# Kernel tuning notes

Hardware: AMD Instinct MI355X
Metric: run time of the kernel (lower is better)

The kernel has to match this reference:

```python
import jax, jax.numpy as jnp
import numpy as np

DIM = 2048
N_HEAD = 32
N_KV = 8
HEAD_DIM = DIM // N_HEAD  # 64
GROUP = N_HEAD // N_KV    # 4


def setup_inputs() -> dict:
    key = jax.random.key(0)
    k1, k2, k3, k4 = jax.random.split(key, 4)
    B, S = 2, 2048
    x = jax.random.normal(k1, (B, S, DIM), dtype=jnp.float32)
    freqs_cis = jax.random.normal(k2, (S, HEAD_DIM // 2, 2), dtype=jnp.float32)
    wqkv_w = jax.random.normal(k3, (DIM, (N_HEAD + 2 * N_KV) * HEAD_DIM), dtype=jnp.float32) * 0.02
    wo_w = jax.random.normal(k4, (DIM, DIM), dtype=jnp.float32) * 0.02
    return {"x": x, "freqs_cis": freqs_cis, "wqkv_w": wqkv_w, "wo_w": wo_w}


def apply_rotary_emb(x, freqs_cis):
    # x: (B, S, H, head_dim), freqs_cis: (S, head_dim//2, 2)
    B, S, H, D = x.shape
    xs = x.astype(jnp.float32).reshape(B, S, H, D // 2, 2)
    fc = freqs_cis.reshape(1, S, 1, D // 2, 2)
    real = xs[..., 0] * fc[..., 0] - xs[..., 1] * fc[..., 1]
    imag = xs[..., 1] * fc[..., 0] + xs[..., 0] * fc[..., 1]
    out = jnp.stack([real, imag], axis=-1).reshape(B, S, H, D)
    return out.astype(x.dtype)


def reference(x, freqs_cis, wqkv_w, wo_w):
    B, S, _ = x.shape
    kv_size = N_KV * HEAD_DIM
    qkv = x @ wqkv_w  # (B, S, (n_head+2*n_kv)*head_dim)
    xq = qkv[..., :DIM].reshape(B, S, N_HEAD, HEAD_DIM)
    xk = qkv[..., DIM:DIM + kv_size].reshape(B, S, N_KV, HEAD_DIM)
    xv = qkv[..., DIM + kv_size:].reshape(B, S, N_KV, HEAD_DIM)

    xq = apply_rotary_emb(xq, freqs_cis)
    xk = apply_rotary_emb(xk, freqs_cis)

    # GQA without materializing repeated KV heads:
    # q: (B, n_kv, group, S, d); k, v: (B, n_kv, S, d)
    q = xq.transpose(0, 2, 1, 3).reshape(B, N_KV, GROUP, S, HEAD_DIM)
    k = xk.transpose(0, 2, 1, 3)
    v = xv.transpose(0, 2, 1, 3)

    scale = 1.0 / jnp.sqrt(jnp.asarray(HEAD_DIM, dtype=q.dtype))
    scores = jnp.einsum('bkgqd,bkKd->bkgqK', q, k) * scale  # (B, n_kv, group, S, S)
    causal = jnp.tril(jnp.ones((S, S), dtype=bool))
    neg = jnp.asarray(jnp.finfo(scores.dtype).min, dtype=scores.dtype)
    scores = jnp.where(causal, scores, neg)
    probs = jax.nn.softmax(scores, axis=-1)
    out = jnp.einsum('bkgqK,bkKd->bkgqd', probs, v)  # (B, n_kv, group, S, d)
    out = out.reshape(B, N_HEAD, S, HEAD_DIM).transpose(0, 2, 1, 3).reshape(B, S, DIM)
    return out @ wo_w
```

## Files before the change

### kernel.cpp

```cpp
#include <hip/hip_runtime.h>
#include <hip/hip_bf16.h>
#include <math.h>

#define DIM 2048
#define NH 32
#define NKV 8
#define HD 64
#define SEQ 2048
#define BATCH 2
#define MTOT (BATCH*SEQ)
#define QKV_N ((NH + 2*NKV)*HD)
#define QSCALE 0.18033688011112042f

typedef __bf16 bf16x8 __attribute__((ext_vector_type(8)));
typedef float f32x4 __attribute__((ext_vector_type(4)));

#if __has_builtin(__builtin_amdgcn_exp2f)
#define EXP2F __builtin_amdgcn_exp2f
#else
#define EXP2F exp2f
#endif

__device__ __forceinline__ void gld_lds16(const void* g, void* l) {
  __builtin_amdgcn_global_load_lds((__attribute__((address_space(1))) void*)g,
                                   (__attribute__((address_space(3))) void*)l,
                                   16, 0, 0);
}

__global__ void cvt_x_kernel(const float* __restrict__ src, __hip_bfloat16* __restrict__ dst, int n4) {
  int i = blockIdx.x * 256 + threadIdx.x;
  if (i >= n4) return;
  float4 v = ((const float4*)src)[i];
  union { __hip_bfloat16 h[4]; uint2 u; } t;
  t.h[0] = __float2bfloat16(v.x); t.h[1] = __float2bfloat16(v.y);
  t.h[2] = __float2bfloat16(v.z); t.h[3] = __float2bfloat16(v.w);
  ((uint2*)dst)[i] = t.u;
}

__global__ void transpose_cvt_kernel(const float* __restrict__ src, __hip_bfloat16* __restrict__ dst,
                                     int R, int C) {
  __shared__ float tile[32][33];
  int c0 = blockIdx.x * 32, r0 = blockIdx.y * 32;
  int tx = threadIdx.x & 31, ty = threadIdx.x >> 5;
  #pragma unroll
  for (int i = ty; i < 32; i += 8)
    tile[i][tx] = src[(size_t)(r0 + i) * C + c0 + tx];
  __syncthreads();
  #pragma unroll
  for (int i = ty; i < 32; i += 8)
    dst[(size_t)(c0 + i) * R + r0 + tx] = __float2bfloat16(tile[tx][i]);
}

__global__ __launch_bounds__(128) void gemm_qkv_rope_kernel(const __hip_bfloat16* __restrict__ A,
                                                            const __hip_bfloat16* __restrict__ Bt,
                                                            const float* __restrict__ freqs,
                                                            __hip_bfloat16* __restrict__ Qb,
                                                            __hip_bfloat16* __restrict__ Kb,
                                                            __hip_bfloat16* __restrict__ Vb) {
  __shared__ __hip_bfloat16 As[64 * 32];
  __shared__ __hip_bfloat16 Bs[128 * 32];
  const int tid = threadIdx.x;
  const int w = tid >> 6, lane = tid & 63, ln = lane & 15, quad = lane >> 4;
  const int id = blockIdx.x;
  const int by = (id & 7) * 8 + ((id >> 3) & 7);
  const int bx = id >> 6;
  const int m0 = by * 64, n0 = bx * 128;
  const int K = DIM;
  const __hip_bfloat16* Ag = A + (size_t)(m0 + w * 32 + (lane >> 2)) * K + (lane & 3) * 8;
  const __hip_bfloat16* Bg = Bt + (size_t)(n0 + w * 64 + (lane >> 2)) * K + (lane & 3) * 8;
  __hip_bfloat16* AsW = &As[w * 1024];
  __hip_bfloat16* BsW = &Bs[w * 2048];
  f32x4 acc[4][4] = {};
  for (int k0 = 0; k0 < K; k0 += 32) {
    gld_lds16(Ag + k0, AsW);
    gld_lds16(Ag + (size_t)16 * K + k0, AsW + 512);
    #pragma unroll
    for (int c = 0; c < 4; c++)
      gld_lds16(Bg + (size_t)(c * 16) * K + k0, BsW + c * 512);
    __syncthreads();
    bf16x8 af[4], bf[4];
    #pragma unroll
    for (int i = 0; i < 4; i++)
      af[i] = *(const bf16x8*)&As[(i * 16 + ln) * 32 + quad * 8];
    #pragma unroll
    for (int j = 0; j < 4; j++)
      bf[j] = *(const bf16x8*)&Bs[(w * 64 + j * 16 + ln) * 32 + quad * 8];
    #pragma unroll
    for (int i = 0; i < 4; i++)
      #pragma unroll
      for (int j = 0; j < 4; j++)
        acc[i][j] = __builtin_amdgcn_mfma_f32_16x16x32_bf16(af[i], bf[j], acc[i][j], 0, 0, 0);
    __syncthreads();
  }
  const int region = (n0 >= 2560) ? 2 : (n0 >= 2048 ? 1 : 0);
  #pragma unroll
  for (int i = 0; i < 4; i++) {
    #pragma unroll
    for (int j = 0; j < 4; j++) {
      const int n = n0 + w * 64 + j * 16 + ln;
      const int d = n & 63;
      #pragma unroll
      for (int r = 0; r < 4; r++) {
        const int m = m0 + i * 16 + quad * 4 + r;
        const int bb = m >> 11, s = m & 2047;
        float v = acc[i][j][r];
        if (region == 2) {
          Vb[((size_t)(bb * NKV + ((n - 2560) >> 6)) * SEQ + s) * HD + d] = __float2bfloat16(v);
        } else {
          float p = __shfl_xor(v, 1);
          const float2 fc = *(const float2*)&freqs[s * 64 + (d & ~1)];
          float o = (d & 1) ? (v * fc.x + p * fc.y) : (v * fc.x - p * fc.y);
          if (region == 0)
            Qb[((size_t)(bb * NH + (n >> 6)) * SEQ + s) * HD + d] = __float2bfloat16(o * QSCALE);
          else
            Kb[((size_t)(bb * NKV + ((n - 2048) >> 6)) * SEQ + s) * HD + d] = __float2bfloat16(o);
        }
      }
    }
  }
}

__global__ __launch_bounds__(128) void gemm_wo_kernel(const __hip_bfloat16* __restrict__ A,
                                                      const __hip_bfloat16* __restrict__ Bt,
                                                      float* __restrict__ C) {
  __shared__ __hip_bfloat16 As[64 * 32];
  __shared__ __hip_bfloat16 Bs[128 * 32];
  const int tid = threadIdx.x;
  const int w = tid >> 6, lane = tid & 63, ln = lane & 15, quad = lane >> 4;
  const int id = blockIdx.x;
  const int by = (id & 7) * 8 + ((id >> 3) & 7);
  const int bx = id >> 6;
  const int m0 = by * 64, n0 = bx * 128;
  const int K = DIM, N = DIM;
  const __hip_bfloat16* Ag = A + (size_t)(m0 + w * 32 + (lane >> 2)) * K + (lane & 3) * 8;
  const __hip_bfloat16* Bg = Bt + (size_t)(n0 + w * 64 + (lane >> 2)) * K + (lane & 3) * 8;
  __hip_bfloat16* AsW = &As[w * 1024];
  __hip_bfloat16* BsW = &Bs[w * 2048];
  f32x4 acc[4][4] = {};
  for (int k0 = 0; k0 < K; k0 += 32) {
    gld_lds16(Ag + k0, AsW);
    gld_lds16(Ag + (size_t)16 * K + k0, AsW + 512);
    #pragma unroll
    for (int c = 0; c < 4; c++)
      gld_lds16(Bg + (size_t)(c * 16) * K + k0, BsW + c * 512);
    __syncthreads();
    bf16x8 af[4], bf[4];
    #pragma unroll
    for (int i = 0; i < 4; i++)
      af[i] = *(const bf16x8*)&As[(i * 16 + ln) * 32 + quad * 8];
    #pragma unroll
    for (int j = 0; j < 4; j++)
      bf[j] = *(const bf16x8*)&Bs[(w * 64 + j * 16 + ln) * 32 + quad * 8];
    #pragma unroll
    for (int i = 0; i < 4; i++)
      #pragma unroll
      for (int j = 0; j < 4; j++)
        acc[i][j] = __builtin_amdgcn_mfma_f32_16x16x32_bf16(af[i], bf[j], acc[i][j], 0, 0, 0);
    __syncthreads();
  }
  #pragma unroll
  for (int i = 0; i < 4; i++) {
    const int r0 = m0 + i * 16 + quad * 4;
    #pragma unroll
    for (int j = 0; j < 4; j++) {
      const int cc = n0 + w * 64 + j * 16 + ln;
      #pragma unroll
      for (int r = 0; r < 4; r++)
        C[(size_t)(r0 + r) * N + cc] = acc[i][j][r];
    }
  }
}

__global__ __launch_bounds__(256, 3) void attn_kernel(const __hip_bfloat16* __restrict__ Q,
                                                      const __hip_bfloat16* __restrict__ Kg,
                                                      const __hip_bfloat16* __restrict__ Vg,
                                                      __hip_bfloat16* __restrict__ O) {
  __shared__ __hip_bfloat16 Ks[128 * 64];
  __shared__ __hip_bfloat16 Vs[64 * 136];
  __shared__ __hip_bfloat16 Ps[4][32 * 72];
  const int id = blockIdx.x;
  const int xcd = id & 7, slot = id >> 3;
  const int cmb = xcd * 2 + (slot >> 6);
  const int b = cmb >> 3, kvh = cmb & 7;
  const int s_ = slot & 63;
  const int t = 15 - (s_ >> 2);
  const int h = kvh * 4 + (s_ & 3);
  const int tid = threadIdx.x, w = tid >> 6, lane = tid & 63, ln = lane & 15, quad = lane >> 4;
  const size_t qbase = (size_t)(b * NH + h) * SEQ * HD;
  const size_t kbase = (size_t)(b * NKV + kvh) * SEQ * HD;

  const __hip_bfloat16* Kgl = Kg + kbase + (size_t)(tid >> 3) * 64 + (size_t)(((tid & 7) ^ ((tid >> 3) & 7)) * 8);
  const int vrow = tid >> 2, vcb = (tid & 3) * 16, vsw = (tid & 3) << 4;
  const int psw = ((ln >> 2) & 3) << 4;

  const int qgw = t * 128 + w * 32;
  bf16x8 qf[2][2];
  #pragma unroll
  for (int f = 0; f < 2; f++)
    #pragma unroll
    for (int kt = 0; kt < 2; kt++)
      qf[f][kt] = *(const bf16x8*)(Q + qbase + (size_t)(qgw + f * 16 + ln) * HD + kt * 32 + quad * 8);
  f32x4 Oacc[2][4] = {};
  float lrow[2][4] = {};
  union { unsigned short u[8]; bf16x8 v; } onesu;
  #pragma unroll
  for (int i = 0; i < 8; i++) onesu.u[i] = 0x3F80;
  const bf16x8 ones = onesu.v;

  uint4 vd[2][2];
  #pragma unroll
  for (int bt = 0; bt < 2; bt++)
    #pragma unroll
    for (int cc = 0; cc < 2; cc++)
      vd[bt][cc] = *(const uint4*)(Vg + kbase + (size_t)(bt * 64 + vrow) * HD + vcb + cc * 8);

  for (int j = 0; j <= t; j++) {
    #pragma unroll
    for (int c = 0; c < 4; c++)
      gld_lds16(Kgl + (size_t)j * 8192 + c * 2048, &Ks[c * 2048 + w * 512]);
    #pragma unroll
    for (int bt = 0; bt < 2; bt++)
      #pragma unroll
      for (int cc = 0; cc < 2; cc++) {
        const __hip_bfloat16* vp = (const __hip_bfloat16*)&vd[bt][cc];
        const int col = vcb + cc * 8;
        const int sr = (bt * 64 + vrow) ^ vsw;
        #pragma unroll
        for (int e = 0; e < 8; e++)
          Vs[(col + e) * 136 + sr] = vp[e];
      }
    __syncthreads();
    if (j < t) {
      #pragma unroll
      for (int bt = 0; bt < 2; bt++)
        #pragma unroll
        for (int cc = 0; cc < 2; cc++)
          vd[bt][cc] = *(const uint4*)(Vg + kbase + (size_t)((j + 1) * 128 + bt * 64 + vrow) * HD + vcb + cc * 8);
    }
    const bool lastIter = (j == t);
    #pragma unroll
    for (int s2 = 0; s2 < 2; s2++) {
      if (lastIter && s2 * 64 > w * 32 + 31) continue;
      bf16x8 kf[4][2];
      #pragma unroll
      for (int nt = 0; nt < 4; nt++)
        #pragma unroll
        for (int kt = 0; kt < 2; kt++) {
          const int kv = s2 * 64 + nt * 16 + ln;
          kf[nt][kt] = *(const bf16x8*)&Ks[(kv * 8 + ((kt * 4 + quad) ^ (ln & 7))) * 8];
        }
      #pragma unroll
      for (int f = 0; f < 2; f++) {
        if (lastIter && s2 * 64 > w * 32 + f * 16 + 15) continue;
        f32x4 sf[4];
        #pragma unroll
        for (int nt = 0; nt < 4; nt++) {
          f32x4 s = {};
          s = __builtin_amdgcn_mfma_f32_16x16x32_bf16(qf[f][0], kf[nt][0], s, 0, 0, 0);
          s = __builtin_amdgcn_mfma_f32_16x16x32_bf16(qf[f][1], kf[nt][1], s, 0, 0, 0);
          sf[nt] = s;
        }
        if (lastIter && s2 * 64 + 63 > w * 32 + f * 16) {
          const int qr = w * 32 + f * 16 + quad * 4;
          #pragma unroll
          for (int nt = 0; nt < 4; nt++) {
            const int kg = s2 * 64 + nt * 16 + ln;
            #pragma unroll
            for (int r = 0; r < 4; r++)
              if (kg > qr + r) sf[nt][r] = -1.0e38f;
          }
        }
        #pragma unroll
        for (int nt = 0; nt < 4; nt++)
          #pragma unroll
          for (int r = 0; r < 4; r++)
            Ps[w][(f * 16 + quad * 4 + r) * 72 + ((nt * 16 + ln) ^ (quad << 4))] =
                __float2bfloat16(EXP2F(sf[nt][r]));
      }
      #pragma unroll
      for (int f = 0; f < 2; f++) {
        if (lastIter && s2 * 64 > w * 32 + f * 16 + 15) continue;
        f32x4 ls = {};
        #pragma unroll
        for (int kt = 0; kt < 2; kt++) {
          bf16x8 pf = *(const bf16x8*)&Ps[w][(f * 16 + ln) * 72 + ((kt * 32 + quad * 8) ^ psw)];
          ls = __builtin_amdgcn_mfma_f32_16x16x32_bf16(pf, ones, ls, 0, 0, 0);
          #pragma unroll
          for (int dt = 0; dt < 4; dt++) {
            bf16x8 vf = *(const bf16x8*)&Vs[(dt * 16 + ln) * 136 + s2 * 64 + ((kt * 32 + quad * 8) ^ (dt << 4))];
            Oacc[f][dt] = __builtin_amdgcn_mfma_f32_16x16x32_bf16(pf, vf, Oacc[f][dt], 0, 0, 0);
          }
        }
        #pragma unroll
        for (int r = 0; r < 4; r++) lrow[f][r] += ls[r];
      }
    }
    __syncthreads();
  }
  #pragma unroll
  for (int f = 0; f < 2; f++) {
    const int so = qgw + f * 16 + quad * 4;
    #pragma unroll
    for (int r = 0; r < 4; r++) {
      const float inv = 1.0f / lrow[f][r];
      #pragma unroll
      for (int dt = 0; dt < 4; dt++)
        O[((size_t)(b * SEQ) + so + r) * DIM + h * HD + dt * 16 + ln] =
            __float2bfloat16(Oacc[f][dt][r] * inv);
    }
  }
}

extern "C" void kernel_launch(void* const* d_in, const int* in_sizes, int n_in,
                              void* d_out, int out_size, void* d_ws, size_t ws_size,
                              hipStream_t stream) {
  const float* x     = (const float*)d_in[0];
  const float* freqs = (const float*)d_in[1];
  const float* wqkv  = (const float*)d_in[2];
  const float* wo    = (const float*)d_in[3];
  float* out = (float*)d_out;

  char* ws = (char*)d_ws;
  __hip_bfloat16* xb    = (__hip_bfloat16*)ws; ws += (size_t)MTOT * DIM * 2;
  __hip_bfloat16* wqkvT = (__hip_bfloat16*)ws; ws += (size_t)QKV_N * DIM * 2;
  __hip_bfloat16* woT   = (__hip_bfloat16*)ws; ws += (size_t)DIM * DIM * 2;
  __hip_bfloat16* Qb    = (__hip_bfloat16*)ws; ws += (size_t)BATCH * NH * SEQ * HD * 2;
  __hip_bfloat16* Kb    = (__hip_bfloat16*)ws; ws += (size_t)BATCH * NKV * SEQ * HD * 2;
  __hip_bfloat16* Vb    = (__hip_bfloat16*)ws; ws += (size_t)BATCH * NKV * SEQ * HD * 2;
  __hip_bfloat16* attnb = (__hip_bfloat16*)ws; ws += (size_t)MTOT * DIM * 2;

  cvt_x_kernel<<<(MTOT * DIM / 4 + 255) / 256, 256, 0, stream>>>(x, xb, MTOT * DIM / 4);
  transpose_cvt_kernel<<<dim3(QKV_N / 32, DIM / 32), 256, 0, stream>>>(wqkv, wqkvT, DIM, QKV_N);
  transpose_cvt_kernel<<<dim3(DIM / 32, DIM / 32), 256, 0, stream>>>(wo, woT, DIM, DIM);
  gemm_qkv_rope_kernel<<<1536, 128, 0, stream>>>(xb, wqkvT, freqs, Qb, Kb, Vb);
  attn_kernel<<<1024, 256, 0, stream>>>(Qb, Kb, Vb, attnb);
  gemm_wo_kernel<<<1024, 128, 0, stream>>>(attnb, woT, out);
}
```

Measured before the change: 364.7 us.

## Replace LDS-staged GEMMs with register-direct single-wave GEMM core with prefetch

Both projection GEMMs drop the shared-memory staging and block barriers. Each single-wavefront block now computes a 64x64 tile by loading MFMA fragments straight from global memory into registers, prefetching the next k-slice while the current MFMAs run. This removes LDS traffic and __syncthreads, but every wave now fetches its own A and B data with no sharing inside the workgroup, so it depends on L2 for reuse. Grid sizes double and the XCD-aware tile mapping changes to match the smaller N tile.

```diff
diff --git a/kernel.cpp b/kernel.cpp
--- a/kernel.cpp
+++ b/kernel.cpp
@@ -51,122 +51,109 @@
     dst[(size_t)(c0 + i) * R + r0 + tx] = __float2bfloat16(tile[tx][i]);
 }
 
-__global__ __launch_bounds__(128) void gemm_qkv_rope_kernel(const __hip_bfloat16* __restrict__ A,
-                                                            const __hip_bfloat16* __restrict__ Bt,
-                                                            const float* __restrict__ freqs,
-                                                            __hip_bfloat16* __restrict__ Qb,
-                                                            __hip_bfloat16* __restrict__ Kb,
-                                                            __hip_bfloat16* __restrict__ Vb) {
-  __shared__ __hip_bfloat16 As[64 * 32];
-  __shared__ __hip_bfloat16 Bs[128 * 32];
-  const int tid = threadIdx.x;
-  const int w = tid >> 6, lane = tid & 63, ln = lane & 15, quad = lane >> 4;
-  const int id = blockIdx.x;
-  const int by = (id & 7) * 8 + ((id >> 3) & 7);
-  const int bx = id >> 6;
-  const int m0 = by * 64, n0 = bx * 128;
-  const int K = DIM;
-  const __hip_bfloat16* Ag = A + (size_t)(m0 + w * 32 + (lane >> 2)) * K + (lane & 3) * 8;
-  const __hip_bfloat16* Bg = Bt + (size_t)(n0 + w * 64 + (lane >> 2)) * K + (lane & 3) * 8;
-  __hip_bfloat16* AsW = &As[w * 1024];
-  __hip_bfloat16* BsW = &Bs[w * 2048];
-  f32x4 acc[4][4] = {};
-  for (int k0 = 0; k0 < K; k0 += 32) {
-    gld_lds16(Ag + k0, AsW);
-    gld_lds16(Ag + (size_t)16 * K + k0, AsW + 512);
-    #pragma unroll
-    for (int c = 0; c < 4; c++)
-      gld_lds16(Bg + (size_t)(c * 16) * K + k0, BsW + c * 512);
-    __syncthreads();
-    bf16x8 af[4], bf[4];
-    #pragma unroll
-    for (int i = 0; i < 4; i++)
-      af[i] = *(const bf16x8*)&As[(i * 16 + ln) * 32 + quad * 8];
-    #pragma unroll
-    for (int j = 0; j < 4; j++)
-      bf[j] = *(const bf16x8*)&Bs[(w * 64 + j * 16 + ln) * 32 + quad * 8];
+__device__ __forceinline__ void gemm_rr_core(const __hip_bfloat16* __restrict__ A,
+                                             const __hip_bfloat16* __restrict__ Bt,
+                                             int m0, int n0, int K, f32x4 (&acc)[4][4]) {
+  const int lane = threadIdx.x & 63, ln = lane & 15, quad = lane >> 4;
+  const __hip_bfloat16* pa[4];
+  const __hip_bfloat16* pb[4];
+  #pragma unroll
+  for (int i = 0; i < 4; i++)
+    pa[i] = A + (size_t)(m0 + i * 16 + ln) * K + quad * 8;
+  #pragma unroll
+  for (int j = 0; j < 4; j++)
+    pb[j] = Bt + (size_t)(n0 + j * 16 + ln) * K + quad * 8;
+
+  bf16x8 af[4], bf[4], an[4], bn[4];
+  #pragma unroll
+  for (int i = 0; i < 4; i++) af[i] = *(const bf16x8*)(pa[i]);
+  #pragma unroll
+  for (int j = 0; j < 4; j++) bf[j] = *(const bf16x8*)(pb[j]);
+
+  for (int k0 = 32; k0 < K; k0 += 32) {
+    #pragma unroll
+    for (int i = 0; i < 4; i++) an[i] = *(const bf16x8*)(pa[i] + k0);
+    #pragma unroll
+    for (int j = 0; j < 4; j++) bn[j] = *(const bf16x8*)(pb[j] + k0);
     #pragma unroll
     for (int i = 0; i < 4; i++)
       #pragma unroll
       for (int j = 0; j < 4; j++)
         acc[i][j] = __builtin_amdgcn_mfma_f32_16x16x32_bf16(af[i], bf[j], acc[i][j], 0, 0, 0);
-    __syncthreads();
-  }
-  const int region = (n0 >= 2560) ? 2 : (n0 >= 2048 ? 1 : 0);
+    #pragma unroll
+    for (int i = 0; i < 4; i++) af[i] = an[i];
+    #pragma unroll
+    for (int j = 0; j < 4; j++) bf[j] = bn[j];
+  }
+  #pragma unroll
+  for (int i = 0; i < 4; i++)
+    #pragma unroll
+    for (int j = 0; j < 4; j++)
+      acc[i][j] = __builtin_amdgcn_mfma_f32_16x16x32_bf16(af[i], bf[j], acc[i][j], 0, 0, 0);
+}
+
+__global__ __launch_bounds__(64, 3) void gemm_qkv_rope_kernel(const __hip_bfloat16* __restrict__ A,
+                                                              const __hip_bfloat16* __restrict__ Bt,
+                                                              const float* __restrict__ freqs,
+                                                              __hip_bfloat16* __restrict__ Qb,
+                                                              __hip_bfloat16* __restrict__ Kb,
+                                                              __hip_bfloat16* __restrict__ Vb) {
+  const int id = blockIdx.x;
+  const int xcd = id & 7, s = id >> 3;
+  const int by = xcd * 8 + (s & 7);
+  const int bx = s >> 3;
+  const int m0 = by * 64, n0 = bx * 64;
+  f32x4 acc[4][4] = {};
+  gemm_rr_core(A, Bt, m0, n0, DIM, acc);
+
+  const int lane = threadIdx.x & 63, ln = lane & 15, quad = lane >> 4;
   #pragma unroll
   for (int i = 0; i < 4; i++) {
     #pragma unroll
     for (int j = 0; j < 4; j++) {
-      const int n = n0 + w * 64 + j * 16 + ln;
-      const int d = n & 63;
+      const int d = j * 16 + ln;
       #pragma unroll
       for (int r = 0; r < 4; r++) {
         const int m = m0 + i * 16 + quad * 4 + r;
-        const int bb = m >> 11, s = m & 2047;
+        const int bb = m >> 11, ss = m & 2047;
         float v = acc[i][j][r];
-        if (region == 2) {
-          Vb[((size_t)(bb * NKV + ((n - 2560) >> 6)) * SEQ + s) * HD + d] = __float2bfloat16(v);
+        if (bx >= 40) {
+          Vb[((size_t)(bb * NKV + (bx - 40)) * SEQ + ss) * HD + d] = __float2bfloat16(v);
         } else {
           float p = __shfl_xor(v, 1);
-          const float2 fc = *(const float2*)&freqs[s * 64 + (d & ~1)];
+          const float2 fc = *(const float2*)&freqs[ss * 64 + (d & ~1)];
           float o = (d & 1) ? (v * fc.x + p * fc.y) : (v * fc.x - p * fc.y);
-          if (region == 0)
-            Qb[((size_t)(bb * NH + (n >> 6)) * SEQ + s) * HD + d] = __float2bfloat16(o * QSCALE);
+          if (bx < 32)
+            Qb[((size_t)(bb * NH + bx) * SEQ + ss) * HD + d] = __float2bfloat16(o * QSCALE);
           else
-            Kb[((size_t)(bb * NKV + ((n - 2048) >> 6)) * SEQ + s) * HD + d] = __float2bfloat16(o);
+            Kb[((size_t)(bb * NKV + (bx - 32)) * SEQ + ss) * HD + d] = __float2bfloat16(o);
         }
       }
     }
   }
 }
 
-__global__ __launch_bounds__(128) void gemm_wo_kernel(const __hip_bfloat16* __restrict__ A,
-                                                      const __hip_bfloat16* __restrict__ Bt,
-                                                      float* __restrict__ C) {
-  __shared__ __hip_bfloat16 As[64 * 32];
-  __shared__ __hip_bfloat16 Bs[128 * 32];
-  const int tid = threadIdx.x;
-  const int w = tid >> 6, lane = tid & 63, ln = lane & 15, quad = lane >> 4;
+__global__ __launch_bounds__(64, 3) void gemm_wo_kernel(const __hip_bfloat16* __restrict__ A,
+                                                        const __hip_bfloat16* __restrict__ Bt,
+                                                        float* __restrict__ C) {
   const int id = blockIdx.x;
-  const int by = (id & 7) * 8 + ((id >> 3) & 7);
-  const int bx = id >> 6;
-  const int m0 = by * 64, n0 = bx * 128;
-  const int K = DIM, N = DIM;
-  const __hip_bfloat16* Ag = A + (size_t)(m0 + w * 32 + (lane >> 2)) * K + (lane & 3) * 8;
-  const __hip_bfloat16* Bg = Bt + (size_t)(n0 + w * 64 + (lane >> 2)) * K + (lane & 3) * 8;
-  __hip_bfloat16* AsW = &As[w * 1024];
-  __hip_bfloat16* BsW = &Bs[w * 2048];
+  const int xcd = id & 7, s = id >> 3;
+  const int by = xcd * 8 + (s & 7);
+  const int bx = s >> 3;
+  const int m0 = by * 64, n0 = bx * 64;
   f32x4 acc[4][4] = {};
-  for (int k0 = 0; k0 < K; k0 += 32) {
-    gld_lds16(Ag + k0, AsW);
-    gld_lds16(Ag + (size_t)16 * K + k0, AsW + 512);
-    #pragma unroll
-    for (int c = 0; c < 4; c++)
-      gld_lds16(Bg + (size_t)(c * 16) * K + k0, BsW + c * 512);
-    __syncthreads();
-    bf16x8 af[4], bf[4];
-    #pragma unroll
-    for (int i = 0; i < 4; i++)
-      af[i] = *(const bf16x8*)&As[(i * 16 + ln) * 32 + quad * 8];
-    #pragma unroll
-    for (int j = 0; j < 4; j++)
-      bf[j] = *(const bf16x8*)&Bs[(w * 64 + j * 16 + ln) * 32 + quad * 8];
-    #pragma unroll
-    for (int i = 0; i < 4; i++)
-      #pragma unroll
-      for (int j = 0; j < 4; j++)
-        acc[i][j] = __builtin_amdgcn_mfma_f32_16x16x32_bf16(af[i], bf[j], acc[i][j], 0, 0, 0);
-    __syncthreads();
-  }
+  gemm_rr_core(A, Bt, m0, n0, DIM, acc);
+
+  const int lane = threadIdx.x & 63, ln = lane & 15, quad = lane >> 4;
   #pragma unroll
   for (int i = 0; i < 4; i++) {
     const int r0 = m0 + i * 16 + quad * 4;
     #pragma unroll
     for (int j = 0; j < 4; j++) {
-      const int cc = n0 + w * 64 + j * 16 + ln;
+      const int cc = n0 + j * 16 + ln;
       #pragma unroll
       for (int r = 0; r < 4; r++)
-        C[(size_t)(r0 + r) * N + cc] = acc[i][j][r];
+        C[(size_t)(r0 + r) * DIM + cc] = acc[i][j][r];
     }
   }
 }
@@ -332,7 +319,7 @@
   cvt_x_kernel<<<(MTOT * DIM / 4 + 255) / 256, 256, 0, stream>>>(x, xb, MTOT * DIM / 4);
   transpose_cvt_kernel<<<dim3(QKV_N / 32, DIM / 32), 256, 0, stream>>>(wqkv, wqkvT, DIM, QKV_N);
   transpose_cvt_kernel<<<dim3(DIM / 32, DIM / 32), 256, 0, stream>>>(wo, woT, DIM, DIM);
-  gemm_qkv_rope_kernel<<<1536, 128, 0, stream>>>(xb, wqkvT, freqs, Qb, Kb, Vb);
+  gemm_qkv_rope_kernel<<<3072, 64, 0, stream>>>(xb, wqkvT, freqs, Qb, Kb, Vb);
   attn_kernel<<<1024, 256, 0, stream>>>(Qb, Kb, Vb, attnb);
-  gemm_wo_kernel<<<1024, 128, 0, stream>>>(attnb, woT, out);
-}
+  gemm_wo_kernel<<<2048, 64, 0, stream>>>(attnb, woT, out);
+}
```

New measurement: 497.1 us. 36.3% more time.
